# Optimization experiments

Measured on AMD Instinct MI355X. Metric: run time of the kernel, lower is better.

The kernel has to match this reference:

```python
import jax, jax.numpy as jnp
import numpy as np

B, N, D = 256, 400, 512
K = 20  # args.gcn_topk == self.k


def setup_inputs() -> dict:
    key = jax.random.key(0)
    k1, k2, k3, k4 = jax.random.split(key, 4)
    node_embs = jax.random.normal(k1, (B, N, D), dtype=jnp.float32)
    h_t = jax.random.normal(k2, (B, D), dtype=jnp.float32)
    mask = jnp.ones((B, N), dtype=jnp.float32)  # unused by forward, kept for signature fidelity
    # mapper = Linear(rnn_dim=512, gcn_dim=512) followed by Tanh
    lim = 1.0 / np.sqrt(D)
    W_map = jax.random.uniform(k3, (D, D), dtype=jnp.float32, minval=-lim, maxval=lim)
    b_map = jax.random.uniform(k4, (D,), dtype=jnp.float32, minval=-lim, maxval=lim)
    return {"node_embs": node_embs, "mask": mask, "h_t": h_t, "W_map": W_map, "b_map": b_map}


def reference(node_embs, mask, h_t, W_map, b_map):
    # scorer = Tanh(Linear(h_t.detach()))  -> [B, D]
    scorer = jnp.tanh(jax.lax.stop_gradient(h_t) @ W_map.T + b_map)
    # scores = bmm(node_embs, scorer) / ||scorer||  -> [B, N]
    scores = jnp.einsum('bnd,bd->bn', node_embs, scorer)
    scores = scores / jnp.linalg.norm(scorer, axis=1, keepdims=True)
    # top-k over nodes
    vals, topk_indices = jax.lax.top_k(scores, K)  # [B, K]
    # vals are always finite => topk_indices_out == topk_indices;
    # repeat_num = K/K + 1 = 2, then truncated back to K => no-op
    topk_indices_out = topk_indices
    # gather rows topk_indices; the original expand(-1,-1,gcn_topk) selects only
    # the FIRST K feature columns -> out is [B, K, K]
    gathered = jnp.take_along_axis(node_embs[:, :, :K], topk_indices[:, :, None], axis=1)
    tanh_s = jnp.tanh(jnp.take_along_axis(scores, topk_indices, axis=1))  # [B, K]
    out = gathered * tanh_s[:, :, None]  # [B, K, K]
    # softmax over nodes, entropy of the categorical, log-prob gather
    logp = jax.nn.log_softmax(scores, axis=1)  # [B, N]
    probs = jnp.exp(logp)
    entropy_object = -jnp.sum(probs * logp, axis=1)  # [B]
    score = jnp.take_along_axis(logp, topk_indices, axis=-1)  # [B, K]
    policy_score = jnp.mean(score, axis=1)  # [B]
    return (jnp.swapaxes(out, 1, 2), policy_score, scorer, entropy_object, topk_indices_out)
```

## Files before the change

### kernel.cpp

```cpp
#include <hip/hip_runtime.h>
#include <math.h>
#include <float.h>

#define BB 256
#define NN 400
#define DD 512
#define KK 20

__device__ __forceinline__ float dot8(float4 a0, float4 a1, float4 b0, float4 b1) {
    return a0.x*b0.x + a0.y*b0.y + a0.z*b0.z + a0.w*b0.w
         + a1.x*b1.x + a1.y*b1.y + a1.z*b1.z + a1.w*b1.w;
}

__global__ __launch_bounds__(1024) void scorer_kernel(
    const float* __restrict__ h_t,
    const float* __restrict__ W,
    const float* __restrict__ bmap,
    float* __restrict__ out2)
{
    const int blk = blockIdx.x;
    const int dc = blk & 15, bg = blk >> 4;
    const int wave = threadIdx.x >> 6, lane = threadIdx.x & 63;

    const int d0 = dc * 32 + wave * 2;
    const int d1 = d0 + 1;
    const float4* wp0 = (const float4*)(W + (size_t)d0 * DD);
    const float4* wp1 = (const float4*)(W + (size_t)d1 * DD);
    const float4 w00 = wp0[lane], w01 = wp0[lane + 64];
    const float4 w10 = wp1[lane], w11 = wp1[lane + 64];
    const float bias0 = bmap[d0], bias1 = bmap[d1];

    #pragma unroll 4
    for (int bi = 0; bi < 32; ++bi) {
        const int b = bg * 32 + bi;
        const float4* hp = (const float4*)(h_t + (size_t)b * DD);
        float4 hb0 = hp[lane], hb1 = hp[lane + 64];
        float p0 = dot8(w00, w01, hb0, hb1);
        float p1 = dot8(w10, w11, hb0, hb1);
        #pragma unroll
        for (int off = 32; off; off >>= 1) {
            p0 += __shfl_xor(p0, off, 64);
            p1 += __shfl_xor(p1, off, 64);
        }
        if (lane == 0) {
            out2[(size_t)b * DD + d0] = tanhf(p0 + bias0);
            out2[(size_t)b * DD + d1] = tanhf(p1 + bias1);
        }
    }
}

__global__ __launch_bounds__(1024, 4) void fused_topk_kernel(
    const float* __restrict__ embs,
    const float* __restrict__ scorer,
    float* __restrict__ out0,
    float* __restrict__ out1,
    float* __restrict__ out3,
    float* __restrict__ out4)
{
    const int b = blockIdx.x;
    const int t = threadIdx.x;
    const int wave = t >> 6, lane = t & 63;

    __shared__ float part[NN][65];
    __shared__ float sh_sc[DD];
    __shared__ float sh_s[NN];
    __shared__ float redf[16], redf2[16], redq[8];
    __shared__ float mZ[3];
    __shared__ int   sh_topk[KK];
    __shared__ float sh_th[KK];

    if (t < DD) {
        float v = scorer[(size_t)b * DD + t];
        sh_sc[t] = v;
        float ss = v * v;
        #pragma unroll
        for (int off = 32; off; off >>= 1) ss += __shfl_xor(ss, off, 64);
        if (lane == 0) redq[wave] = ss;
    }
    __syncthreads();

    const float4 g0 = ((const float4*)sh_sc)[lane];
    const float4 g1 = ((const float4*)sh_sc)[lane + 64];

    {
        const int n0 = wave * 25;
        const float* rowbase = embs + ((size_t)b * NN + n0) * DD;
        for (int g = 0; g < 5; ++g) {
            float4 A0[5], A1[5];
            #pragma unroll
            for (int r = 0; r < 5; ++r) {
                const float4* p = (const float4*)(rowbase + (size_t)(g * 5 + r) * DD);
                A0[r] = p[lane];
                A1[r] = p[lane + 64];
            }
            #pragma unroll
            for (int r = 0; r < 5; ++r)
                part[n0 + g * 5 + r][lane] = dot8(A0[r], A1[r], g0, g1);
        }
    }
    __syncthreads();

    if (t == 0) {
        float tot = 0.f;
        #pragma unroll
        for (int i = 0; i < 8; ++i) tot += redq[i];
        mZ[0] = 1.0f / sqrtf(tot);
    }

    float raw = 0.f;
    if (t < NN) {
        const float* pr = part[t];
        float a0 = 0.f, a1 = 0.f, a2 = 0.f, a3 = 0.f;
        #pragma unroll
        for (int i = 0; i < 64; i += 4) {
            a0 += pr[i]; a1 += pr[i + 1]; a2 += pr[i + 2]; a3 += pr[i + 3];
        }
        raw = (a0 + a1) + (a2 + a3);
        sh_s[t] = raw;
    }
    __syncthreads();
    const float inv = mZ[0];

    const float x = (t < NN) ? raw * inv : -FLT_MAX;
    {
        float m = x;
        #pragma unroll
        for (int off = 32; off; off >>= 1) m = fmaxf(m, __shfl_xor(m, off, 64));
        if (lane == 0) redf[wave] = m;
    }
    __syncthreads();
    if (t == 0) {
        float m = redf[0];
        #pragma unroll
        for (int i = 1; i < 16; ++i) m = fmaxf(m, redf[i]);
        mZ[1] = m;
    }
    __syncthreads();
    const float m = mZ[1];

    {
        float e = 0.f, wv = 0.f;
        if (t < NN) {
            float d = x - m;
            e = expf(d);
            wv = e * d;
        }
        #pragma unroll
        for (int off = 32; off; off >>= 1) {
            e  += __shfl_xor(e, off, 64);
            wv += __shfl_xor(wv, off, 64);
        }
        if (lane == 0) { redf[wave] = e; redf2[wave] = wv; }
    }
    __syncthreads();
    if (t == 0) {
        float Z = 0.f, Ws = 0.f;
        #pragma unroll
        for (int i = 0; i < 16; ++i) { Z += redf[i]; Ws += redf2[i]; }
        float logZ = logf(Z);
        mZ[2] = logZ;
        out3[b] = logZ - Ws / Z;
    }
    __syncthreads();
    const float logZ = mZ[2];

    if (wave == 0) {
        float v0 = sh_s[lane      ] * inv;
        float v1 = sh_s[lane +  64] * inv;
        float v2 = sh_s[lane + 128] * inv;
        float v3 = sh_s[lane + 192] * inv;
        float v4 = sh_s[lane + 256] * inv;
        float v5 = sh_s[lane + 320] * inv;
        float v6 = (lane + 384 < NN) ? sh_s[lane + 384] * inv : -FLT_MAX;
        float acc = 0.f;
        for (int k = 0; k < KK; ++k) {
            float bv = v0; int bi = lane;
            if (v1 > bv) { bv = v1; bi = lane + 64; }
            if (v2 > bv) { bv = v2; bi = lane + 128; }
            if (v3 > bv) { bv = v3; bi = lane + 192; }
            if (v4 > bv) { bv = v4; bi = lane + 256; }
            if (v5 > bv) { bv = v5; bi = lane + 320; }
            if (v6 > bv) { bv = v6; bi = lane + 384; }
            #pragma unroll
            for (int off = 32; off; off >>= 1) {
                float ov = __shfl_xor(bv, off, 64);
                int   oi = __shfl_xor(bi, off, 64);
                if (ov > bv || (ov == bv && oi < bi)) { bv = ov; bi = oi; }
            }
            if (lane == 0) {
                sh_topk[k] = bi;
                sh_th[k] = tanhf(bv);
                out4[(size_t)b * KK + k] = (float)bi;
                acc += bv - m - logZ;
            }
            v0 = (bi == lane      ) ? -FLT_MAX : v0;
            v1 = (bi == lane +  64) ? -FLT_MAX : v1;
            v2 = (bi == lane + 128) ? -FLT_MAX : v2;
            v3 = (bi == lane + 192) ? -FLT_MAX : v3;
            v4 = (bi == lane + 256) ? -FLT_MAX : v4;
            v5 = (bi == lane + 320) ? -FLT_MAX : v5;
            v6 = (bi == lane + 384) ? -FLT_MAX : v6;
        }
        if (lane == 0) out1[b] = acc / (float)KK;
    }
    __syncthreads();

    if (t < NN) {
        int k = t / KK;
        int j = t - k * KK;
        float val = embs[((size_t)b * NN + sh_topk[k]) * DD + j] * sh_th[k];
        out0[(size_t)b * (KK * KK) + j * KK + k] = val;
    }
}

extern "C" void kernel_launch(void* const* d_in, const int* in_sizes, int n_in,
                              void* d_out, int out_size, void* d_ws, size_t ws_size,
                              hipStream_t stream) {
    const float* node_embs = (const float*)d_in[0];
    const float* h_t   = (const float*)d_in[2];
    const float* W_map = (const float*)d_in[3];
    const float* b_map = (const float*)d_in[4];
    (void)d_ws; (void)ws_size; (void)in_sizes; (void)n_in; (void)out_size;

    float* ob = (float*)d_out;
    float* out0 = ob;
    float* out1 = ob + 102400;
    float* out2 = ob + 102656;
    float* out3 = ob + 233728;
    float* out4 = ob + 233984;

    scorer_kernel<<<128, 1024, 0, stream>>>(h_t, W_map, b_map, out2);
    fused_topk_kernel<<<BB, 1024, 0, stream>>>(node_embs, out2, out0, out1, out3, out4);
}
```

Baseline: 74.26 us.

## Split fused top-k kernel into a wide scores pass and a small finalize pass

The single per-batch 1024-thread kernel, which used a large shared-memory partial-sum array, is split into two kernels. A bandwidth-bound scores kernel runs 4 blocks per batch row with 256 threads each and reduces dot products with wave shuffles instead of shared memory. A 512-thread finalize kernel handles softmax, entropy, top-k and the gather. The aim is higher occupancy and better memory parallelism for streaming the 200MB embedding tensor, at the cost of an extra launch and a workspace round trip for the raw scores.

```diff
diff --git a/kernel.cpp b/kernel.cpp
--- a/kernel.cpp
+++ b/kernel.cpp
@@ -49,9 +49,55 @@
     }
 }
 
-__global__ __launch_bounds__(1024, 4) void fused_topk_kernel(
+__global__ __launch_bounds__(256, 4) void scores_kernel(
     const float* __restrict__ embs,
     const float* __restrict__ scorer,
+    float* __restrict__ raw)
+{
+    const int blk = blockIdx.x;
+    const int b = blk >> 2, q = blk & 3;
+    const int wave = threadIdx.x >> 6, lane = threadIdx.x & 63;
+
+    const float4* sp = (const float4*)(scorer + (size_t)b * DD);
+    const float4 g0 = sp[lane];
+    const float4 g1 = sp[lane + 64];
+
+    const int n0 = q * 100 + wave * 25;
+    const float* base = embs + ((size_t)b * NN + n0) * DD;
+
+    #pragma unroll
+    for (int g = 0; g < 5; ++g) {
+        float4 A0[5], A1[5];
+        #pragma unroll
+        for (int r = 0; r < 5; ++r) {
+            const float4* p = (const float4*)(base + (size_t)(g * 5 + r) * DD);
+            A0[r] = p[lane];
+            A1[r] = p[lane + 64];
+        }
+        float s0 = dot8(A0[0], A1[0], g0, g1);
+        float s1 = dot8(A0[1], A1[1], g0, g1);
+        float s2 = dot8(A0[2], A1[2], g0, g1);
+        float s3 = dot8(A0[3], A1[3], g0, g1);
+        float s4 = dot8(A0[4], A1[4], g0, g1);
+        #pragma unroll
+        for (int off = 32; off; off >>= 1) {
+            s0 += __shfl_xor(s0, off, 64);
+            s1 += __shfl_xor(s1, off, 64);
+            s2 += __shfl_xor(s2, off, 64);
+            s3 += __shfl_xor(s3, off, 64);
+            s4 += __shfl_xor(s4, off, 64);
+        }
+        if (lane == 0) {
+            float* o = raw + (size_t)b * NN + n0 + g * 5;
+            o[0] = s0; o[1] = s1; o[2] = s2; o[3] = s3; o[4] = s4;
+        }
+    }
+}
+
+__global__ __launch_bounds__(512) void finalize_kernel(
+    const float* __restrict__ embs,
+    const float* __restrict__ scorer,
+    const float* __restrict__ raw,
     float* __restrict__ out0,
     float* __restrict__ out1,
     float* __restrict__ out3,
@@ -61,67 +107,33 @@
     const int t = threadIdx.x;
     const int wave = t >> 6, lane = t & 63;
 
-    __shared__ float part[NN][65];
-    __shared__ float sh_sc[DD];
     __shared__ float sh_s[NN];
-    __shared__ float redf[16], redf2[16], redq[8];
+    __shared__ float redf[8], redf2[8];
     __shared__ float mZ[3];
     __shared__ int   sh_topk[KK];
     __shared__ float sh_th[KK];
 
-    if (t < DD) {
+    {
         float v = scorer[(size_t)b * DD + t];
-        sh_sc[t] = v;
         float ss = v * v;
         #pragma unroll
         for (int off = 32; off; off >>= 1) ss += __shfl_xor(ss, off, 64);
-        if (lane == 0) redq[wave] = ss;
-    }
-    __syncthreads();
-
-    const float4 g0 = ((const float4*)sh_sc)[lane];
-    const float4 g1 = ((const float4*)sh_sc)[lane + 64];
-
-    {
-        const int n0 = wave * 25;
-        const float* rowbase = embs + ((size_t)b * NN + n0) * DD;
-        for (int g = 0; g < 5; ++g) {
-            float4 A0[5], A1[5];
-            #pragma unroll
-            for (int r = 0; r < 5; ++r) {
-                const float4* p = (const float4*)(rowbase + (size_t)(g * 5 + r) * DD);
-                A0[r] = p[lane];
-                A1[r] = p[lane + 64];
-            }
-            #pragma unroll
-            for (int r = 0; r < 5; ++r)
-                part[n0 + g * 5 + r][lane] = dot8(A0[r], A1[r], g0, g1);
-        }
-    }
-    __syncthreads();
-
+        if (lane == 0) redf[wave] = ss;
+    }
+    const float rawv = (t < NN) ? raw[(size_t)b * NN + t] : 0.f;
+    __syncthreads();
     if (t == 0) {
         float tot = 0.f;
         #pragma unroll
-        for (int i = 0; i < 8; ++i) tot += redq[i];
+        for (int i = 0; i < 8; ++i) tot += redf[i];
         mZ[0] = 1.0f / sqrtf(tot);
     }
-
-    float raw = 0.f;
-    if (t < NN) {
-        const float* pr = part[t];
-        float a0 = 0.f, a1 = 0.f, a2 = 0.f, a3 = 0.f;
-        #pragma unroll
-        for (int i = 0; i < 64; i += 4) {
-            a0 += pr[i]; a1 += pr[i + 1]; a2 += pr[i + 2]; a3 += pr[i + 3];
-        }
-        raw = (a0 + a1) + (a2 + a3);
-        sh_s[t] = raw;
-    }
     __syncthreads();
     const float inv = mZ[0];
 
-    const float x = (t < NN) ? raw * inv : -FLT_MAX;
+    const float x = (t < NN) ? rawv * inv : -FLT_MAX;
+    if (t < NN) sh_s[t] = x;
+
     {
         float m = x;
         #pragma unroll
@@ -132,7 +144,7 @@
     if (t == 0) {
         float m = redf[0];
         #pragma unroll
-        for (int i = 1; i < 16; ++i) m = fmaxf(m, redf[i]);
+        for (int i = 1; i < 8; ++i) m = fmaxf(m, redf[i]);
         mZ[1] = m;
     }
     __syncthreads();
@@ -156,7 +168,7 @@
     if (t == 0) {
         float Z = 0.f, Ws = 0.f;
         #pragma unroll
-        for (int i = 0; i < 16; ++i) { Z += redf[i]; Ws += redf2[i]; }
+        for (int i = 0; i < 8; ++i) { Z += redf[i]; Ws += redf2[i]; }
         float logZ = logf(Z);
         mZ[2] = logZ;
         out3[b] = logZ - Ws / Z;
@@ -165,13 +177,13 @@
     const float logZ = mZ[2];
 
     if (wave == 0) {
-        float v0 = sh_s[lane      ] * inv;
-        float v1 = sh_s[lane +  64] * inv;
-        float v2 = sh_s[lane + 128] * inv;
-        float v3 = sh_s[lane + 192] * inv;
-        float v4 = sh_s[lane + 256] * inv;
-        float v5 = sh_s[lane + 320] * inv;
-        float v6 = (lane + 384 < NN) ? sh_s[lane + 384] * inv : -FLT_MAX;
+        float v0 = sh_s[lane      ];
+        float v1 = sh_s[lane +  64];
+        float v2 = sh_s[lane + 128];
+        float v3 = sh_s[lane + 192];
+        float v4 = sh_s[lane + 256];
+        float v5 = sh_s[lane + 320];
+        float v6 = (lane + 384 < NN) ? sh_s[lane + 384] : -FLT_MAX;
         float acc = 0.f;
         for (int k = 0; k < KK; ++k) {
             float bv = v0; int bi = lane;
@@ -220,7 +232,7 @@
     const float* h_t   = (const float*)d_in[2];
     const float* W_map = (const float*)d_in[3];
     const float* b_map = (const float*)d_in[4];
-    (void)d_ws; (void)ws_size; (void)in_sizes; (void)n_in; (void)out_size;
+    (void)in_sizes; (void)n_in; (void)out_size; (void)ws_size;
 
     float* ob = (float*)d_out;
     float* out0 = ob;
@@ -229,6 +241,10 @@
     float* out3 = ob + 233728;
     float* out4 = ob + 233984;
 
+    float* raw_scores = (float*)d_ws;
+
     scorer_kernel<<<128, 1024, 0, stream>>>(h_t, W_map, b_map, out2);
-    fused_topk_kernel<<<BB, 1024, 0, stream>>>(node_embs, out2, out0, out1, out3, out4);
-}
+    scores_kernel<<<BB * 4, 256, 0, stream>>>(node_embs, out2, raw_scores);
+    finalize_kernel<<<BB, 512, 0, stream>>>(node_embs, out2, raw_scores,
+                                            out0, out1, out3, out4);
+}
```

New measurement: 75.77 us. 1.02x slower.

## Double-buffer embedding row loads and reduce dot products with wave shuffles

Applied to the files above, without the earlier changes.

The score computation now prefetches the next group of five rows into a second register set while the current group is processed, overlapping global loads with compute. The large 400x65 shared-memory partial-sum array is replaced by an in-register shuffle reduction per row, with lane 0 writing the final score. This removes about 100KB of LDS and a full pass of partial-sum reads, which may allow more blocks per CU. The cost is higher register pressure from the extra buffers and more shuffle instructions.

```diff
diff --git a/kernel.cpp b/kernel.cpp
--- a/kernel.cpp
+++ b/kernel.cpp
@@ -61,7 +61,6 @@
     const int t = threadIdx.x;
     const int wave = t >> 6, lane = t & 63;
 
-    __shared__ float part[NN][65];
     __shared__ float sh_sc[DD];
     __shared__ float sh_s[NN];
     __shared__ float redf[16], redf2[16], redq[8];
@@ -84,18 +83,40 @@
 
     {
         const int n0 = wave * 25;
-        const float* rowbase = embs + ((size_t)b * NN + n0) * DD;
+        const float* base = embs + ((size_t)b * NN + n0) * DD;
+
+        float4 A0[5], A1[5], B0[5], B1[5];
+        #pragma unroll
+        for (int r = 0; r < 5; ++r) {
+            const float4* p = (const float4*)(base + (size_t)r * DD);
+            A0[r] = p[lane]; A1[r] = p[lane + 64];
+        }
+        #pragma unroll
         for (int g = 0; g < 5; ++g) {
-            float4 A0[5], A1[5];
+            if (g < 4) {
+                #pragma unroll
+                for (int r = 0; r < 5; ++r) {
+                    const float4* p = (const float4*)(base + (size_t)((g + 1) * 5 + r) * DD);
+                    B0[r] = p[lane]; B1[r] = p[lane + 64];
+                }
+            }
+            float s[5];
             #pragma unroll
-            for (int r = 0; r < 5; ++r) {
-                const float4* p = (const float4*)(rowbase + (size_t)(g * 5 + r) * DD);
-                A0[r] = p[lane];
-                A1[r] = p[lane + 64];
-            }
+            for (int r = 0; r < 5; ++r) s[r] = dot8(A0[r], A1[r], g0, g1);
             #pragma unroll
-            for (int r = 0; r < 5; ++r)
-                part[n0 + g * 5 + r][lane] = dot8(A0[r], A1[r], g0, g1);
+            for (int off = 32; off; off >>= 1) {
+                #pragma unroll
+                for (int r = 0; r < 5; ++r) s[r] += __shfl_xor(s[r], off, 64);
+            }
+            if (lane == 0) {
+                float* o = sh_s + n0 + g * 5;
+                #pragma unroll
+                for (int r = 0; r < 5; ++r) o[r] = s[r];
+            }
+            if (g < 4) {
+                #pragma unroll
+                for (int r = 0; r < 5; ++r) { A0[r] = B0[r]; A1[r] = B1[r]; }
+            }
         }
     }
     __syncthreads();
@@ -106,22 +127,10 @@
         for (int i = 0; i < 8; ++i) tot += redq[i];
         mZ[0] = 1.0f / sqrtf(tot);
     }
-
-    float raw = 0.f;
-    if (t < NN) {
-        const float* pr = part[t];
-        float a0 = 0.f, a1 = 0.f, a2 = 0.f, a3 = 0.f;
-        #pragma unroll
-        for (int i = 0; i < 64; i += 4) {
-            a0 += pr[i]; a1 += pr[i + 1]; a2 += pr[i + 2]; a3 += pr[i + 3];
-        }
-        raw = (a0 + a1) + (a2 + a3);
-        sh_s[t] = raw;
-    }
     __syncthreads();
     const float inv = mZ[0];
 
-    const float x = (t < NN) ? raw * inv : -FLT_MAX;
+    const float x = (t < NN) ? sh_s[t] * inv : -FLT_MAX;
     {
         float m = x;
         #pragma unroll
@@ -220,7 +229,7 @@
     const float* h_t   = (const float*)d_in[2];
     const float* W_map = (const float*)d_in[3];
     const float* b_map = (const float*)d_in[4];
-    (void)d_ws; (void)ws_size; (void)in_sizes; (void)n_in; (void)out_size;
+    (void)in_sizes; (void)n_in; (void)out_size; (void)d_ws; (void)ws_size;
 
     float* ob = (float*)d_out;
     float* out0 = ob;
@@ -230,5 +239,6 @@
     float* out4 = ob + 233984;
 
     scorer_kernel<<<128, 1024, 0, stream>>>(h_t, W_map, b_map, out2);
-    fused_topk_kernel<<<BB, 1024, 0, stream>>>(node_embs, out2, out0, out1, out3, out4);
-}
+    fused_topk_kernel<<<BB, 1024, 0, stream>>>(node_embs, out2,
+                                               out0, out1, out3, out4);
+}
```

Measured after the change: 73.45 us. About the same (-1.1%).
